# Performance work log

Hardware: AMD Instinct MI355X
Metric: run time of the kernel (lower is better)

Reference implementation:

```python
import jax, jax.numpy as jnp
import numpy as np

B, S, D = 2, 2048, 1024
H, Dh = 16, 64  # qkv_features=1024, head_dim=64
F = 1024        # out_features


def setup_inputs() -> dict:
    key = jax.random.key(0)
    ks = jax.random.split(key, 16)
    s = 0.02
    return {
        'inputs_q': jax.random.normal(ks[0], (B, S, D), jnp.float32),
        'inputs_kv': jax.random.normal(ks[1], (B, S, D), jnp.float32),
        'pos_embed': jax.random.normal(ks[2], (S, D), jnp.float32),
        'Wq': jax.random.normal(ks[3], (D, H, Dh), jnp.float32) * s,
        'bq': jnp.zeros((H, Dh), jnp.float32),
        'Wk': jax.random.normal(ks[4], (D, H, Dh), jnp.float32) * s,
        'bk': jnp.zeros((H, Dh), jnp.float32),
        'Wv': jax.random.normal(ks[5], (D, H, Dh), jnp.float32) * s,
        'bv': jnp.zeros((H, Dh), jnp.float32),
        'Wpos': jax.random.normal(ks[6], (D, H, Dh), jnp.float32) * s,
        'r_r_bias': jax.random.normal(ks[7], (H, Dh), jnp.float32) * s,
        'r_w_bias': jax.random.normal(ks[8], (H, Dh), jnp.float32) * s,
        'Wout': jax.random.normal(ks[9], (H, Dh, F), jnp.float32) * s,
        'bout': jnp.zeros((F,), jnp.float32),
    }


_roll_vmap = jax.vmap(jnp.roll, in_axes=(-2, 0, None), out_axes=-2)


def reference(inputs_q, inputs_kv, pos_embed, Wq, bq, Wk, bk, Wv, bv,
              Wpos, r_r_bias, r_w_bias, Wout, bout):
    # QKV projections: [B,S,D] x [D,H,Dh] -> [B,S,H,Dh]
    q = jnp.einsum('bsd,dhk->bshk', inputs_q, Wq) + bq
    k = jnp.einsum('bsd,dhk->bshk', inputs_kv, Wk) + bk
    v = jnp.einsum('bsd,dhk->bshk', inputs_kv, Wv) + bv
    # relative position embedding projection: [S,D] -> [S,H,Dh]
    r_pos = jnp.einsum('sd,dhk->shk', pos_embed, Wpos)

    q_len = q.shape[-3]
    depth = q.shape[-1]
    # content score + relative-position score, both [B,H,S,S]
    aw = jnp.einsum('bqhd,bkhd->bhqk', q + r_w_bias, k)
    aw_r = jnp.einsum('bqhd,khd->bhqk', q + r_r_bias, r_pos)
    # Transformer-XL relative shift: per query-row roll along key axis
    shifts = jnp.arange(0, q_len) - (q_len - 1)
    aw_r = _roll_vmap(aw_r, shifts, -1)
    aw = (aw + aw_r) / jnp.sqrt(depth).astype(aw.dtype)
    attn = jax.nn.softmax(aw, axis=-1)
    # weighted sum: [B,S,H,Dh]
    x = jnp.einsum('bhqk,bkhd->bqhd', attn, v)
    # output projection contracting (H,Dh)
    out = jnp.einsum('bqhd,hdf->bqf', x, Wout) + bout
    return out
```

## Files before the change

kernel.cpp:

```cpp
#include <hip/hip_runtime.h>
#include <hip/hip_bf16.h>
#include <hip/hip_fp16.h>


#define B_  2
#define S_  2048
#define D_  1024
#define H_  16
#define DH_ 64
#define HD_ 1024
#define F_  1024
#define N_  4096
#define KC_ 512
#define SP2 520

typedef __attribute__((ext_vector_type(8))) short  short8;
typedef __attribute__((ext_vector_type(4))) float  floatx4;

__device__ __forceinline__ unsigned short f2bf(float x) {
  unsigned u = __float_as_uint(x);
  u += 0x7FFFu + ((u >> 16) & 1u);
  return (unsigned short)(u >> 16);
}
__device__ __forceinline__ unsigned short f2h(float x) {
  __half h = __float2half(x);
  unsigned short u; __builtin_memcpy(&u, &h, 2);
  return u;
}
__device__ __forceinline__ float h2f(unsigned short u) {
  __half h; __builtin_memcpy(&h, &u, 2);
  return __half2float(h);
}

#define CQ_ (N_ * D_ / 4)
__global__ void cast_all(const float* __restrict__ sq, const float* __restrict__ skv,
                         const float* __restrict__ spos,
                         unsigned short* __restrict__ dq, unsigned short* __restrict__ dkv,
                         unsigned short* __restrict__ dpos) {
  int i = blockIdx.x * blockDim.x + threadIdx.x;
  const float* s; unsigned short* d; int off;
  if (i < CQ_)            { s = sq;   d = dq;   off = i; }
  else if (i < 2 * CQ_)   { s = skv;  d = dkv;  off = i - CQ_; }
  else                    { s = spos; d = dpos; off = i - 2 * CQ_; }
  float4 v = ((const float4*)s)[off];
  ushort4 o = make_ushort4(f2bf(v.x), f2bf(v.y), f2bf(v.z), f2bf(v.w));
  ((ushort4*)d)[off] = o;
}

struct TP5 { const float* s[5]; unsigned short* d[5]; };
__global__ void transpose_all(TP5 p) {
  __shared__ float t[32][33];
  const float* src = p.s[blockIdx.z];
  unsigned short* dst = p.d[blockIdx.z];
  int c0 = blockIdx.x * 32, r0 = blockIdx.y * 32;
  int tx = threadIdx.x, ty = threadIdx.y;
#pragma unroll
  for (int i = 0; i < 4; i++)
    t[ty + i * 8][tx] = src[(size_t)(r0 + ty + i * 8) * 1024 + c0 + tx];
  __syncthreads();
#pragma unroll
  for (int i = 0; i < 4; i++)
    dst[(size_t)(c0 + ty + i * 8) * 1024 + r0 + tx] = f2bf(t[tx][ty + i * 8]);
}

__launch_bounds__(256, 2)
__global__ void gemm_bt(const unsigned short* A, const unsigned short* Bt,
                        const float* bias, const float* b2a, const float* b2b,
                        unsigned short* outA, unsigned short* outB, float* outF,
                        int Nn, int K, int mode, int split,
                        const unsigned short* A2, const unsigned short* Bt2,
                        const float* bias2, unsigned short* outA2, int mode2) {
  __shared__ unsigned short As[128 * 64];
  __shared__ unsigned short Bs[128 * 64];
  int bx = blockIdx.x;
  if (split && bx >= split) {
    bx -= split; A = A2; Bt = Bt2; bias = bias2; outA = outA2; mode = mode2;
    b2a = nullptr; b2b = nullptr;
  }
  int nb = Nn >> 7;
  int bm = bx / nb, bn = bx % nb;
  int tid = threadIdx.x;
  int lane = tid & 63, wv = tid >> 6;
  int wm = wv >> 1, wn = wv & 1;
  int lm = lane & 15, lg = lane >> 4;
  const unsigned short* Ab = A + (size_t)(bm * 128) * K;
  const unsigned short* Bb = Bt + (size_t)(bn * 128) * K;
  floatx4 acc[4][4];
#pragma unroll
  for (int i = 0; i < 4; i++)
#pragma unroll
    for (int j = 0; j < 4; j++) acc[i][j] = (floatx4){0.f, 0.f, 0.f, 0.f};

  int lr = tid >> 3;
  int lc = (tid & 7) * 8;
  for (int k0 = 0; k0 < K; k0 += 64) {
    __syncthreads();
#pragma unroll
    for (int i = 0; i < 4; i++) {
      int r = i * 32 + lr;
      *(uint4*)&As[r * 64 + lc] = *(const uint4*)&Ab[(size_t)r * K + k0 + lc];
      *(uint4*)&Bs[r * 64 + lc] = *(const uint4*)&Bb[(size_t)r * K + k0 + lc];
    }
    __syncthreads();
#pragma unroll
    for (int kk = 0; kk < 2; kk++) {
      short8 af[4], bf[4];
#pragma unroll
      for (int i = 0; i < 4; i++)
        af[i] = *(const short8*)&As[(wm * 64 + i * 16 + lm) * 64 + kk * 32 + lg * 8];
#pragma unroll
      for (int j = 0; j < 4; j++)
        bf[j] = *(const short8*)&Bs[(wn * 64 + j * 16 + lm) * 64 + kk * 32 + lg * 8];
#pragma unroll
      for (int i = 0; i < 4; i++)
#pragma unroll
        for (int j = 0; j < 4; j++)
          acc[i][j] = __builtin_amdgcn_mfma_f32_16x16x32_bf16(af[i], bf[j], acc[i][j], 0, 0, 0);
    }
  }
#pragma unroll
  for (int j = 0; j < 4; j++) {
    int col = bn * 128 + wn * 64 + j * 16 + lm;
    float bs = bias ? bias[col] : 0.f;
    float ba = b2a ? b2a[col] : 0.f;
    float bb = b2b ? b2b[col] : 0.f;
#pragma unroll
    for (int i = 0; i < 4; i++) {
      int row0 = bm * 128 + wm * 64 + i * 16 + lg * 4;
      if (mode == 4) {
        int s = row0 & 2047, bb2 = row0 >> 11;
        size_t vidx = (((size_t)bb2 * H_ + (col >> 6)) * 64 + (col & 63)) * (size_t)S_ + s;
        ushort4 o = make_ushort4(f2bf(acc[i][j][0] + bs), f2bf(acc[i][j][1] + bs),
                                 f2bf(acc[i][j][2] + bs), f2bf(acc[i][j][3] + bs));
        *(ushort4*)&outA[vidx] = o;
      } else {
#pragma unroll
        for (int r = 0; r < 4; r++) {
          float v = acc[i][j][r] + bs;
          size_t idx = (size_t)(row0 + r) * Nn + col;
          if (mode == 0)      outA[idx] = f2bf(v);
          else if (mode == 1) { outA[idx] = f2bf(v + ba); outB[idx] = f2bf(v + bb); }
          else                outF[idx] = v;
        }
      }
    }
  }
}

__launch_bounds__(512, 4)
__global__ void attn_kernel(const unsigned short* __restrict__ qw,
                            const unsigned short* __restrict__ qr,
                            const unsigned short* __restrict__ kb,
                            const unsigned short* __restrict__ rb,
                            const unsigned short* __restrict__ vt,
                            unsigned short* __restrict__ xb) {
  __shared__ __align__(16) unsigned short sS[2][32 * SP2];
  __shared__ float sSum[8][32];
  __shared__ float sLinv[32];
  int bid = blockIdx.x;
  int qt = bid & 63;
  int bh = bid >> 6;
  int b = bh >> 4, h = bh & 15;
  int q0 = qt * 32;
  int tid = threadIdx.x;
  int lane = tid & 63, wv = tid >> 6;
  int lm = lane & 15, lg = lane >> 4;

  short8 bqw[2][2], bqr[2][2];
  const size_t qbase = (size_t)(b * S_ + q0) * HD_ + h * 64;
#pragma unroll
  for (int t = 0; t < 2; t++) {
    const unsigned short* p1 = qw + qbase + (size_t)(t * 16 + lm) * HD_ + lg * 8;
    const unsigned short* p2 = qr + qbase + (size_t)(t * 16 + lm) * HD_ + lg * 8;
    bqw[t][0] = *(const short8*)(p1);
    bqw[t][1] = *(const short8*)(p1 + 32);
    bqr[t][0] = *(const short8*)(p2);
    bqr[t][1] = *(const short8*)(p2 + 32);
  }

  floatx4 acc[2][4];
#pragma unroll
  for (int m = 0; m < 2; m++)
#pragma unroll
    for (int j = 0; j < 4; j++) acc[m][j] = (floatx4){0.f, 0.f, 0.f, 0.f};
  float s0 = 0.f, s1 = 0.f;

  const unsigned short* vb0 = vt + (size_t)(b * H_ + h) * 64 * S_;
  const float KSC = 0.1803368801111204f;

  for (int c = 0; c < 4; c++) {
    unsigned short* S = sS[c & 1];
    int kc = c * KC_;
    for (int jt = wv; jt < 34; jt += 8) {
      int jrow = (kc - q0 - 32 + jt * 16 + lm) & 2047;
      const unsigned short* rp = rb + (size_t)jrow * HD_ + h * 64 + lg * 8;
      short8 a0 = *(const short8*)(rp);
      short8 a1 = *(const short8*)(rp + 32);
#pragma unroll
      for (int t = 0; t < 2; t++) {
        floatx4 c4 = (floatx4){0.f, 0.f, 0.f, 0.f};
        c4 = __builtin_amdgcn_mfma_f32_16x16x32_bf16(a0, bqr[t][0], c4, 0, 0, 0);
        c4 = __builtin_amdgcn_mfma_f32_16x16x32_bf16(a1, bqr[t][1], c4, 0, 0, 0);
        int q = t * 16 + lm;
        int ub = jt * 16 + lg * 4 + q - 31;
        unsigned short* row = &S[q * SP2];
#pragma unroll
        for (int r = 0; r < 4; r++) {
          int u = ub + r;
          if ((unsigned)u < (unsigned)KC_) row[u] = f2h(c4[r]);
        }
      }
    }
    __syncthreads();
#pragma unroll 2
    for (int kt = 0; kt < 4; kt++) {
      int u0 = wv * 64 + kt * 16;
      const unsigned short* kp = kb + (size_t)(b * S_ + kc + u0 + lm) * HD_ + h * 64 + lg * 8;
      short8 a0 = *(const short8*)(kp);
      short8 a1 = *(const short8*)(kp + 32);
#pragma unroll
      for (int t = 0; t < 2; t++) {
        floatx4 c4 = (floatx4){0.f, 0.f, 0.f, 0.f};
        c4 = __builtin_amdgcn_mfma_f32_16x16x32_bf16(a0, bqw[t][0], c4, 0, 0, 0);
        c4 = __builtin_amdgcn_mfma_f32_16x16x32_bf16(a1, bqw[t][1], c4, 0, 0, 0);
        int q = t * 16 + lm;
        ushort4* p = (ushort4*)&S[q * SP2 + u0 + lg * 4];
        ushort4 Rv = *p;
        float p0 = exp2f((c4[0] + h2f(Rv.x)) * KSC);
        float p1 = exp2f((c4[1] + h2f(Rv.y)) * KSC);
        float p2 = exp2f((c4[2] + h2f(Rv.z)) * KSC);
        float p3 = exp2f((c4[3] + h2f(Rv.w)) * KSC);
        float ps = (p0 + p1) + (p2 + p3);
        if (t == 0) s0 += ps; else s1 += ps;
        *p = make_ushort4(f2bf(p0), f2bf(p1), f2bf(p2), f2bf(p3));
      }
    }
    __syncthreads();
#pragma unroll
    for (int s = 0; s < 2; s++) {
      int u0 = wv * 64 + s * 32;
      short8 a0 = *(short8*)&S[lm * SP2 + u0 + lg * 8];
      short8 a1 = *(short8*)&S[(16 + lm) * SP2 + u0 + lg * 8];
      const unsigned short* vp = vb0 + kc + u0 + lg * 8;
#pragma unroll
      for (int j = 0; j < 4; j++) {
        short8 bb = *(const short8*)&vp[(size_t)(j * 16 + lm) * S_];
        acc[0][j] = __builtin_amdgcn_mfma_f32_16x16x32_bf16(a0, bb, acc[0][j], 0, 0, 0);
        acc[1][j] = __builtin_amdgcn_mfma_f32_16x16x32_bf16(a1, bb, acc[1][j], 0, 0, 0);
      }
    }
  }
  s0 += __shfl_xor(s0, 16); s0 += __shfl_xor(s0, 32);
  s1 += __shfl_xor(s1, 16); s1 += __shfl_xor(s1, 32);
  if (lane < 16) { sSum[wv][lane] = s0; sSum[wv][16 + lane] = s1; }
  __syncthreads();
  if (tid < 32) {
    float t = 0.f;
#pragma unroll
    for (int w = 0; w < 8; w++) t += sSum[w][tid];
    sLinv[tid] = 1.f / t;
  }
  float* po = (float*)sS;
#pragma unroll
  for (int m = 0; m < 2; m++)
#pragma unroll
    for (int j = 0; j < 4; j++)
#pragma unroll
      for (int r = 0; r < 4; r++) {
        int q = m * 16 + lg * 4 + r;
        int dh = j * 16 + lm;
        po[wv * 2048 + q * 64 + dh] = acc[m][j][r];
      }
  __syncthreads();
  {
    int e = tid * 4;
    int q = e >> 6, dh = e & 63;
    float4 v = *(float4*)&po[e];
#pragma unroll
    for (int w = 1; w < 8; w++) {
      float4 u = *(float4*)&po[w * 2048 + e];
      v.x += u.x; v.y += u.y; v.z += u.z; v.w += u.w;
    }
    float li = sLinv[q];
    ushort4 o = make_ushort4(f2bf(v.x * li), f2bf(v.y * li), f2bf(v.z * li), f2bf(v.w * li));
    *(ushort4*)&xb[(size_t)(b * S_ + q0 + q) * HD_ + h * 64 + dh] = o;
  }
}

extern "C" void kernel_launch(void* const* d_in, const int* in_sizes, int n_in,
                              void* d_out, int out_size, void* d_ws, size_t ws_size,
                              hipStream_t stream) {
  const float* inputs_q  = (const float*)d_in[0];
  const float* inputs_kv = (const float*)d_in[1];
  const float* pos_embed = (const float*)d_in[2];
  const float* Wq   = (const float*)d_in[3];
  const float* bq   = (const float*)d_in[4];
  const float* Wk   = (const float*)d_in[5];
  const float* bk   = (const float*)d_in[6];
  const float* Wv   = (const float*)d_in[7];
  const float* bv   = (const float*)d_in[8];
  const float* Wpos = (const float*)d_in[9];
  const float* rrb  = (const float*)d_in[10];
  const float* rwb  = (const float*)d_in[11];
  const float* Wout = (const float*)d_in[12];
  const float* bout = (const float*)d_in[13];
  float* out = (float*)d_out;

  char* ws = (char*)d_ws;
  unsigned short* aq  = (unsigned short*)(ws);
  unsigned short* akv = (unsigned short*)(ws + ( 8u << 20));
  unsigned short* apo = (unsigned short*)(ws + (16u << 20));
  unsigned short* wqt = (unsigned short*)(ws + (20u << 20));
  unsigned short* wkt = (unsigned short*)(ws + (22u << 20));
  unsigned short* wvt = (unsigned short*)(ws + (24u << 20));
  unsigned short* wpt = (unsigned short*)(ws + (26u << 20));
  unsigned short* wot = (unsigned short*)(ws + (28u << 20));
  unsigned short* qwp = (unsigned short*)(ws + (30u << 20));
  unsigned short* qrp = (unsigned short*)(ws + (38u << 20));
  unsigned short* kbp = (unsigned short*)(ws + (46u << 20));
  unsigned short* vtp = (unsigned short*)(ws + (54u << 20));
  unsigned short* rbp = (unsigned short*)(ws + (62u << 20));
  unsigned short* xbp = aq;

  cast_all<<<10240, 256, 0, stream>>>(inputs_q, inputs_kv, pos_embed, aq, akv, apo);
  TP5 tp;
  tp.s[0] = Wq; tp.s[1] = Wk; tp.s[2] = Wv; tp.s[3] = Wpos; tp.s[4] = Wout;
  tp.d[0] = wqt; tp.d[1] = wkt; tp.d[2] = wvt; tp.d[3] = wpt; tp.d[4] = wot;
  transpose_all<<<dim3(32, 32, 5), dim3(32, 8), 0, stream>>>(tp);

  gemm_bt<<<256 + 128, 256, 0, stream>>>(aq, wqt, bq, rwb, rrb, qwp, qrp, nullptr,
                                         HD_, D_, 1, 256, apo, wpt, nullptr, rbp, 0);
  gemm_bt<<<512, 256, 0, stream>>>(akv, wkt, bk, nullptr, nullptr, kbp, nullptr, nullptr,
                                   HD_, D_, 0, 256, akv, wvt, bv, vtp, 4);
  attn_kernel<<<2048, 512, 0, stream>>>(qwp, qrp, kbp, rbp, vtp, xbp);
  gemm_bt<<<256, 256, 0, stream>>>(xbp, wot, bout, nullptr, nullptr, nullptr, nullptr, out,
                                   F_, HD_, 2, 0, nullptr, nullptr, nullptr, nullptr, 0);
}
```

Measured before the change: 431.2 us.

## Keep softmax probabilities in registers and swizzle V layout to match MFMA operands

The softmax probabilities now stay in registers, packed to bf16 with v_cvt_pk_bf16_f32. They feed the PV MFMA directly instead of being written back to shared memory and reloaded, which drops one __syncthreads per chunk. To make the register layout line up with the MFMA operand, the V-transpose store permutes sequence indices within each 32-block. The softmax scale moves into the Q projection epilogue, and part of the K fragments are prefetched before the relative-position phase. The shared-memory row pitch shrinks and bounds checks on interior tiles are skipped. The risks are wrong permutation mapping, higher register pressure, and slight bf16 rounding differences from pre-scaling Q.

```diff
diff --git a/kernel.cpp b/kernel.cpp
--- a/kernel.cpp
+++ b/kernel.cpp
@@ -12,10 +12,12 @@
 #define F_  1024
 #define N_  4096
 #define KC_ 512
-#define SP2 520
+#define SP2 516
+#define KQSC 0.1803368801111204f
 
 typedef __attribute__((ext_vector_type(8))) short  short8;
 typedef __attribute__((ext_vector_type(4))) float  floatx4;
+typedef __attribute__((ext_vector_type(4))) unsigned int uintx4;
 
 __device__ __forceinline__ unsigned short f2bf(float x) {
   unsigned u = __float_as_uint(x);
@@ -129,7 +131,8 @@
       int row0 = bm * 128 + wm * 64 + i * 16 + lg * 4;
       if (mode == 4) {
         int s = row0 & 2047, bb2 = row0 >> 11;
-        size_t vidx = (((size_t)bb2 * H_ + (col >> 6)) * 64 + (col & 63)) * (size_t)S_ + s;
+        int sw = (s & ~31) | ((s & 12) << 1) | ((s & 16) >> 2) | (s & 3);
+        size_t vidx = (((size_t)bb2 * H_ + (col >> 6)) * 64 + (col & 63)) * (size_t)S_ + sw;
         ushort4 o = make_ushort4(f2bf(acc[i][j][0] + bs), f2bf(acc[i][j][1] + bs),
                                  f2bf(acc[i][j][2] + bs), f2bf(acc[i][j][3] + bs));
         *(ushort4*)&outA[vidx] = o;
@@ -139,7 +142,7 @@
           float v = acc[i][j][r] + bs;
           size_t idx = (size_t)(row0 + r) * Nn + col;
           if (mode == 0)      outA[idx] = f2bf(v);
-          else if (mode == 1) { outA[idx] = f2bf(v + ba); outB[idx] = f2bf(v + bb); }
+          else if (mode == 1) { outA[idx] = f2bf((v + ba) * KQSC); outB[idx] = f2bf((v + bb) * KQSC); }
           else                outF[idx] = v;
         }
       }
@@ -186,11 +189,17 @@
   float s0 = 0.f, s1 = 0.f;
 
   const unsigned short* vb0 = vt + (size_t)(b * H_ + h) * 64 * S_;
-  const float KSC = 0.1803368801111204f;
 
   for (int c = 0; c < 4; c++) {
     unsigned short* S = sS[c & 1];
     int kc = c * KC_;
+    short8 ka[2][2];
+#pragma unroll
+    for (int kt = 0; kt < 2; kt++) {
+      const unsigned short* kp = kb + (size_t)(b * S_ + kc + wv * 64 + kt * 16 + lm) * HD_ + h * 64 + lg * 8;
+      ka[kt][0] = *(const short8*)(kp);
+      ka[kt][1] = *(const short8*)(kp + 32);
+    }
     for (int jt = wv; jt < 34; jt += 8) {
       int jrow = (kc - q0 - 32 + jt * 16 + lm) & 2047;
       const unsigned short* rp = rb + (size_t)jrow * HD_ + h * 64 + lg * 8;
@@ -204,49 +213,60 @@
         int q = t * 16 + lm;
         int ub = jt * 16 + lg * 4 + q - 31;
         unsigned short* row = &S[q * SP2];
-#pragma unroll
-        for (int r = 0; r < 4; r++) {
-          int u = ub + r;
-          if ((unsigned)u < (unsigned)KC_) row[u] = f2h(c4[r]);
+        if (jt + t >= 2 && jt + t <= 32) {
+#pragma unroll
+          for (int r = 0; r < 4; r++) row[ub + r] = f2h(c4[r]);
+        } else {
+#pragma unroll
+          for (int r = 0; r < 4; r++) {
+            int u = ub + r;
+            if ((unsigned)u < (unsigned)KC_) row[u] = f2h(c4[r]);
+          }
         }
       }
     }
     __syncthreads();
-#pragma unroll 2
+    uintx4 pw[2][2];
+#pragma unroll
     for (int kt = 0; kt < 4; kt++) {
+      short8 a0, a1;
+      if (kt < 2) { a0 = ka[kt][0]; a1 = ka[kt][1]; }
+      else {
+        const unsigned short* kp = kb + (size_t)(b * S_ + kc + wv * 64 + kt * 16 + lm) * HD_ + h * 64 + lg * 8;
+        a0 = *(const short8*)(kp);
+        a1 = *(const short8*)(kp + 32);
+      }
       int u0 = wv * 64 + kt * 16;
-      const unsigned short* kp = kb + (size_t)(b * S_ + kc + u0 + lm) * HD_ + h * 64 + lg * 8;
-      short8 a0 = *(const short8*)(kp);
-      short8 a1 = *(const short8*)(kp + 32);
 #pragma unroll
       for (int t = 0; t < 2; t++) {
         floatx4 c4 = (floatx4){0.f, 0.f, 0.f, 0.f};
         c4 = __builtin_amdgcn_mfma_f32_16x16x32_bf16(a0, bqw[t][0], c4, 0, 0, 0);
         c4 = __builtin_amdgcn_mfma_f32_16x16x32_bf16(a1, bqw[t][1], c4, 0, 0, 0);
         int q = t * 16 + lm;
-        ushort4* p = (ushort4*)&S[q * SP2 + u0 + lg * 4];
-        ushort4 Rv = *p;
-        float p0 = exp2f((c4[0] + h2f(Rv.x)) * KSC);
-        float p1 = exp2f((c4[1] + h2f(Rv.y)) * KSC);
-        float p2 = exp2f((c4[2] + h2f(Rv.z)) * KSC);
-        float p3 = exp2f((c4[3] + h2f(Rv.w)) * KSC);
+        ushort4 Rv = *(const ushort4*)&S[q * SP2 + u0 + lg * 4];
+        float p0 = exp2f(c4[0] + h2f(Rv.x));
+        float p1 = exp2f(c4[1] + h2f(Rv.y));
+        float p2 = exp2f(c4[2] + h2f(Rv.z));
+        float p3 = exp2f(c4[3] + h2f(Rv.w));
         float ps = (p0 + p1) + (p2 + p3);
         if (t == 0) s0 += ps; else s1 += ps;
-        *p = make_ushort4(f2bf(p0), f2bf(p1), f2bf(p2), f2bf(p3));
-      }
-    }
-    __syncthreads();
+        unsigned w0, w1;
+        asm("v_cvt_pk_bf16_f32 %0, %1, %2" : "=v"(w0) : "v"(p0), "v"(p1));
+        asm("v_cvt_pk_bf16_f32 %0, %1, %2" : "=v"(w1) : "v"(p2), "v"(p3));
+        pw[t][kt >> 1][(kt & 1) * 2]     = w0;
+        pw[t][kt >> 1][(kt & 1) * 2 + 1] = w1;
+      }
+    }
 #pragma unroll
     for (int s = 0; s < 2; s++) {
-      int u0 = wv * 64 + s * 32;
-      short8 a0 = *(short8*)&S[lm * SP2 + u0 + lg * 8];
-      short8 a1 = *(short8*)&S[(16 + lm) * SP2 + u0 + lg * 8];
-      const unsigned short* vp = vb0 + kc + u0 + lg * 8;
+      short8 pa0 = __builtin_bit_cast(short8, pw[0][s]);
+      short8 pa1 = __builtin_bit_cast(short8, pw[1][s]);
+      const unsigned short* vp = vb0 + kc + wv * 64 + s * 32 + lg * 8;
 #pragma unroll
       for (int j = 0; j < 4; j++) {
         short8 bb = *(const short8*)&vp[(size_t)(j * 16 + lm) * S_];
-        acc[0][j] = __builtin_amdgcn_mfma_f32_16x16x32_bf16(a0, bb, acc[0][j], 0, 0, 0);
-        acc[1][j] = __builtin_amdgcn_mfma_f32_16x16x32_bf16(a1, bb, acc[1][j], 0, 0, 0);
+        acc[0][j] = __builtin_amdgcn_mfma_f32_16x16x32_bf16(pa0, bb, acc[0][j], 0, 0, 0);
+        acc[1][j] = __builtin_amdgcn_mfma_f32_16x16x32_bf16(pa1, bb, acc[1][j], 0, 0, 0);
       }
     }
   }
```

Result: slower. 512.3 us (+18.8%).

## Merge projection GEMMs, fold softmax scale into Q, trim attention sync and LDS traffic

Applied to the files above, without the earlier changes.

The Q/pos GEMM launch and the K/V GEMM launch become one 896-block launch, driven by a segment table passed as a kernel argument. The softmax scale (log2e/sqrt(d)) is applied in the Q projection epilogue, which removes a multiply per score in attention. In the attention kernel, the block index is swizzled so neighbouring blocks work on different heads. The barrier between the exp phase and the PV phase is dropped, since each wave reads only the P columns it wrote. Smaller changes: the LDS row pitch goes from 520 to 516, interior rel-pos stores skip the bounds check, bf16 packing uses v_cvt_pk_bf16_f32, and P is loaded as 8-byte pieces because of the new pitch. Risks include bank conflicts or misaligned access from the 516 pitch, and rounding differences from scaling Q before the bf16 cast.

```diff
diff --git a/kernel.cpp b/kernel.cpp
--- a/kernel.cpp
+++ b/kernel.cpp
@@ -12,10 +12,12 @@
 #define F_  1024
 #define N_  4096
 #define KC_ 512
-#define SP2 520
+#define SP2 516
+#define KQSC 0.1803368801111204f
 
 typedef __attribute__((ext_vector_type(8))) short  short8;
 typedef __attribute__((ext_vector_type(4))) float  floatx4;
+typedef __attribute__((ext_vector_type(4))) unsigned int uintx4;
 
 __device__ __forceinline__ unsigned short f2bf(float x) {
   unsigned u = __float_as_uint(x);
@@ -63,28 +65,31 @@
     dst[(size_t)(c0 + ty + i * 8) * 1024 + r0 + tx] = f2bf(t[tx][ty + i * 8]);
 }
 
+struct GSeg {
+  const unsigned short* A; const unsigned short* Bt;
+  const float* bias; const float* b2a; const float* b2b;
+  unsigned short* outA; unsigned short* outB; float* outF;
+  int mode; int bend;
+};
+struct GP { GSeg s[4]; };
 __launch_bounds__(256, 2)
-__global__ void gemm_bt(const unsigned short* A, const unsigned short* Bt,
-                        const float* bias, const float* b2a, const float* b2b,
-                        unsigned short* outA, unsigned short* outB, float* outF,
-                        int Nn, int K, int mode, int split,
-                        const unsigned short* A2, const unsigned short* Bt2,
-                        const float* bias2, unsigned short* outA2, int mode2) {
+__global__ void gemm_bt(GP p, int Nn, int K) {
   __shared__ unsigned short As[128 * 64];
   __shared__ unsigned short Bs[128 * 64];
   int bx = blockIdx.x;
-  if (split && bx >= split) {
-    bx -= split; A = A2; Bt = Bt2; bias = bias2; outA = outA2; mode = mode2;
-    b2a = nullptr; b2b = nullptr;
-  }
+  GSeg g = p.s[0]; int base = 0;
+  if (bx >= p.s[0].bend) { g = p.s[1]; base = p.s[0].bend; }
+  if (bx >= p.s[1].bend) { g = p.s[2]; base = p.s[1].bend; }
+  if (bx >= p.s[2].bend) { g = p.s[3]; base = p.s[2].bend; }
+  bx -= base;
   int nb = Nn >> 7;
   int bm = bx / nb, bn = bx % nb;
   int tid = threadIdx.x;
   int lane = tid & 63, wv = tid >> 6;
   int wm = wv >> 1, wn = wv & 1;
   int lm = lane & 15, lg = lane >> 4;
-  const unsigned short* Ab = A + (size_t)(bm * 128) * K;
-  const unsigned short* Bb = Bt + (size_t)(bn * 128) * K;
+  const unsigned short* Ab = g.A + (size_t)(bm * 128) * K;
+  const unsigned short* Bb = g.Bt + (size_t)(bn * 128) * K;
   floatx4 acc[4][4];
 #pragma unroll
   for (int i = 0; i < 4; i++)
@@ -121,26 +126,26 @@
 #pragma unroll
   for (int j = 0; j < 4; j++) {
     int col = bn * 128 + wn * 64 + j * 16 + lm;
-    float bs = bias ? bias[col] : 0.f;
-    float ba = b2a ? b2a[col] : 0.f;
-    float bb = b2b ? b2b[col] : 0.f;
+    float bs = g.bias ? g.bias[col] : 0.f;
+    float ba = g.b2a ? g.b2a[col] : 0.f;
+    float bb = g.b2b ? g.b2b[col] : 0.f;
 #pragma unroll
     for (int i = 0; i < 4; i++) {
       int row0 = bm * 128 + wm * 64 + i * 16 + lg * 4;
-      if (mode == 4) {
+      if (g.mode == 4) {
         int s = row0 & 2047, bb2 = row0 >> 11;
         size_t vidx = (((size_t)bb2 * H_ + (col >> 6)) * 64 + (col & 63)) * (size_t)S_ + s;
         ushort4 o = make_ushort4(f2bf(acc[i][j][0] + bs), f2bf(acc[i][j][1] + bs),
                                  f2bf(acc[i][j][2] + bs), f2bf(acc[i][j][3] + bs));
-        *(ushort4*)&outA[vidx] = o;
+        *(ushort4*)&g.outA[vidx] = o;
       } else {
 #pragma unroll
         for (int r = 0; r < 4; r++) {
           float v = acc[i][j][r] + bs;
           size_t idx = (size_t)(row0 + r) * Nn + col;
-          if (mode == 0)      outA[idx] = f2bf(v);
-          else if (mode == 1) { outA[idx] = f2bf(v + ba); outB[idx] = f2bf(v + bb); }
-          else                outF[idx] = v;
+          if (g.mode == 0)      g.outA[idx] = f2bf(v);
+          else if (g.mode == 1) { g.outA[idx] = f2bf((v + ba) * KQSC); g.outB[idx] = f2bf((v + bb) * KQSC); }
+          else                  g.outF[idx] = v;
         }
       }
     }
@@ -158,8 +163,9 @@
   __shared__ float sSum[8][32];
   __shared__ float sLinv[32];
   int bid = blockIdx.x;
-  int qt = bid & 63;
-  int bh = bid >> 6;
+  int l = ((bid & 7) << 8) | (bid >> 3);
+  int qt = l & 63;
+  int bh = l >> 6;
   int b = bh >> 4, h = bh & 15;
   int q0 = qt * 32;
   int tid = threadIdx.x;
@@ -186,7 +192,6 @@
   float s0 = 0.f, s1 = 0.f;
 
   const unsigned short* vb0 = vt + (size_t)(b * H_ + h) * 64 * S_;
-  const float KSC = 0.1803368801111204f;
 
   for (int c = 0; c < 4; c++) {
     unsigned short* S = sS[c & 1];
@@ -204,10 +209,15 @@
         int q = t * 16 + lm;
         int ub = jt * 16 + lg * 4 + q - 31;
         unsigned short* row = &S[q * SP2];
-#pragma unroll
-        for (int r = 0; r < 4; r++) {
-          int u = ub + r;
-          if ((unsigned)u < (unsigned)KC_) row[u] = f2h(c4[r]);
+        if (jt + t >= 2 && jt + t <= 32) {
+#pragma unroll
+          for (int r = 0; r < 4; r++) row[ub + r] = f2h(c4[r]);
+        } else {
+#pragma unroll
+          for (int r = 0; r < 4; r++) {
+            int u = ub + r;
+            if ((unsigned)u < (unsigned)KC_) row[u] = f2h(c4[r]);
+          }
         }
       }
     }
@@ -224,23 +234,33 @@
         c4 = __builtin_amdgcn_mfma_f32_16x16x32_bf16(a0, bqw[t][0], c4, 0, 0, 0);
         c4 = __builtin_amdgcn_mfma_f32_16x16x32_bf16(a1, bqw[t][1], c4, 0, 0, 0);
         int q = t * 16 + lm;
-        ushort4* p = (ushort4*)&S[q * SP2 + u0 + lg * 4];
-        ushort4 Rv = *p;
-        float p0 = exp2f((c4[0] + h2f(Rv.x)) * KSC);
-        float p1 = exp2f((c4[1] + h2f(Rv.y)) * KSC);
-        float p2 = exp2f((c4[2] + h2f(Rv.z)) * KSC);
-        float p3 = exp2f((c4[3] + h2f(Rv.w)) * KSC);
+        unsigned short* pp = &S[q * SP2 + u0 + lg * 4];
+        ushort4 Rv = *(const ushort4*)pp;
+        float p0 = exp2f(c4[0] + h2f(Rv.x));
+        float p1 = exp2f(c4[1] + h2f(Rv.y));
+        float p2 = exp2f(c4[2] + h2f(Rv.z));
+        float p3 = exp2f(c4[3] + h2f(Rv.w));
         float ps = (p0 + p1) + (p2 + p3);
         if (t == 0) s0 += ps; else s1 += ps;
-        *p = make_ushort4(f2bf(p0), f2bf(p1), f2bf(p2), f2bf(p3));
-      }
-    }
-    __syncthreads();
+        unsigned w0, w1;
+        asm("v_cvt_pk_bf16_f32 %0, %1, %2" : "=v"(w0) : "v"(p0), "v"(p1));
+        asm("v_cvt_pk_bf16_f32 %0, %1, %2" : "=v"(w1) : "v"(p2), "v"(p3));
+        *(uint2*)pp = make_uint2(w0, w1);
+      }
+    }
 #pragma unroll
     for (int s = 0; s < 2; s++) {
       int u0 = wv * 64 + s * 32;
-      short8 a0 = *(short8*)&S[lm * SP2 + u0 + lg * 8];
-      short8 a1 = *(short8*)&S[(16 + lm) * SP2 + u0 + lg * 8];
+      int e0 = lm * SP2 + u0 + lg * 8;
+      int e1 = (16 + lm) * SP2 + u0 + lg * 8;
+      uint2 x0 = *(const uint2*)&S[e0];
+      uint2 x1 = *(const uint2*)&S[e0 + 4];
+      uint2 y0 = *(const uint2*)&S[e1];
+      uint2 y1 = *(const uint2*)&S[e1 + 4];
+      uintx4 ua = {x0.x, x0.y, x1.x, x1.y};
+      uintx4 ub = {y0.x, y0.y, y1.x, y1.y};
+      short8 a0 = __builtin_bit_cast(short8, ua);
+      short8 a1 = __builtin_bit_cast(short8, ub);
       const unsigned short* vp = vb0 + kc + u0 + lg * 8;
 #pragma unroll
       for (int j = 0; j < 4; j++) {
@@ -328,11 +348,19 @@
   tp.d[0] = wqt; tp.d[1] = wkt; tp.d[2] = wvt; tp.d[3] = wpt; tp.d[4] = wot;
   transpose_all<<<dim3(32, 32, 5), dim3(32, 8), 0, stream>>>(tp);
 
-  gemm_bt<<<256 + 128, 256, 0, stream>>>(aq, wqt, bq, rwb, rrb, qwp, qrp, nullptr,
-                                         HD_, D_, 1, 256, apo, wpt, nullptr, rbp, 0);
-  gemm_bt<<<512, 256, 0, stream>>>(akv, wkt, bk, nullptr, nullptr, kbp, nullptr, nullptr,
-                                   HD_, D_, 0, 256, akv, wvt, bv, vtp, 4);
+  GP gp{};
+  gp.s[0] = {aq,  wqt, bq,      rwb,     rrb,     qwp,     qrp,     nullptr, 1, 256};
+  gp.s[1] = {apo, wpt, nullptr, nullptr, nullptr, rbp,     nullptr, nullptr, 0, 384};
+  gp.s[2] = {akv, wkt, bk,      nullptr, nullptr, kbp,     nullptr, nullptr, 0, 640};
+  gp.s[3] = {akv, wvt, bv,      nullptr, nullptr, vtp,     nullptr, nullptr, 4, 896};
+  gemm_bt<<<896, 256, 0, stream>>>(gp, HD_, D_);
+
   attn_kernel<<<2048, 512, 0, stream>>>(qwp, qrp, kbp, rbp, vtp, xbp);
-  gemm_bt<<<256, 256, 0, stream>>>(xbp, wot, bout, nullptr, nullptr, nullptr, nullptr, out,
-                                   F_, HD_, 2, 0, nullptr, nullptr, nullptr, nullptr, 0);
-}
+
+  GP go{};
+  go.s[0] = {xbp, wot, bout, nullptr, nullptr, nullptr, nullptr, out, 2, 256};
+  go.s[1] = {nullptr, nullptr, nullptr, nullptr, nullptr, nullptr, nullptr, nullptr, 0, 1 << 30};
+  go.s[2] = go.s[1];
+  go.s[3] = go.s[1];
+  gemm_bt<<<256, 256, 0, stream>>>(go, F_, HD_);
+}
```

After: 405.9 us. -5.9%, faster.
